# Optimization experiments

Hardware: AMD Instinct MI355X
Metric: run time of the kernel (lower is better)

## Reference

```python
import jax, jax.numpy as jnp
import numpy as np
import math

D_MODEL = 1024
N_HEAD = 16
B, T = 4, 2048


def setup_inputs() -> dict:
    key = jax.random.key(0)
    ks = jax.random.split(key, 12)
    s = 1.0 / math.sqrt(D_MODEL)
    inp = {
        "q": jax.random.normal(ks[0], (B, T, D_MODEL), dtype=jnp.float32),
        "k": jax.random.normal(ks[1], (B, T, D_MODEL), dtype=jnp.float32),
        "v": jax.random.normal(ks[2], (B, T, D_MODEL), dtype=jnp.float32),
        "Wq": jax.random.uniform(ks[3], (D_MODEL, D_MODEL), jnp.float32, -s, s),
        "bq": jax.random.uniform(ks[4], (D_MODEL,), jnp.float32, -s, s),
        "Wk": jax.random.uniform(ks[5], (D_MODEL, D_MODEL), jnp.float32, -s, s),
        "bk": jax.random.uniform(ks[6], (D_MODEL,), jnp.float32, -s, s),
        "Wv": jax.random.uniform(ks[7], (D_MODEL, D_MODEL), jnp.float32, -s, s),
        "bv": jax.random.uniform(ks[8], (D_MODEL,), jnp.float32, -s, s),
        "Wo": jax.random.uniform(ks[9], (D_MODEL, D_MODEL), jnp.float32, -s, s),
        "bo": jax.random.uniform(ks[10], (D_MODEL,), jnp.float32, -s, s),
    }
    return inp


def reference(q, k, v, Wq, bq, Wk, bk, Wv, bv, Wo, bo):
    # NOTE: original module applies all three projections to `q` (k, v args unused)
    batch, time, dim = q.shape
    n_d = dim // N_HEAD
    # torch Linear: x @ W.T + b
    Q = (q @ Wq.T + bq).reshape(batch, time, N_HEAD, n_d).transpose(0, 2, 1, 3)
    K = (q @ Wk.T + bk).reshape(batch, time, N_HEAD, n_d).transpose(0, 2, 1, 3)
    V = (q @ Wv.T + bv).reshape(batch, time, N_HEAD, n_d).transpose(0, 2, 1, 3)
    # [B, H, T, T]
    score = jnp.einsum("bhqd,bhkd->bhqk", Q, K) / jnp.sqrt(jnp.float32(n_d))
    causal = jnp.tril(jnp.ones((time, time), dtype=bool))
    score = jnp.where(causal, score, -jnp.inf)
    # original uses Softmax(dim=-2): normalizes over the QUERY axis (faithful)
    attn = jax.nn.softmax(score, axis=-2)
    ctx = jnp.einsum("bhqk,bhkd->bhqd", attn, V)
    ctx = ctx.transpose(0, 2, 1, 3).reshape(batch, time, dim)
    return ctx @ Wo.T + bo
```

## Files before the change

### kernel.cpp

```cpp
#include <hip/hip_runtime.h>
#include <hip/hip_bf16.h>
#include <cstdint>
#include <cstddef>

typedef __bf16 bf16x8 __attribute__((ext_vector_type(8)));
typedef __bf16 bf16x4 __attribute__((ext_vector_type(4)));
typedef __bf16 bf16x2 __attribute__((ext_vector_type(2)));
typedef float  f32x4  __attribute__((ext_vector_type(4)));

static constexpr int TSEQ  = 2048;
static constexpr int DM    = 1024;
static constexpr int NH    = 16;
static constexpr int HD    = 64;
static constexpr int BATCH = 4;
static constexpr float SCL = 0.18033688011112042f;

__device__ __forceinline__ void gload16(const __bf16* g, __bf16* l) {
  __builtin_amdgcn_global_load_lds((const __attribute__((address_space(1))) void*)g,
                                   (__attribute__((address_space(3))) void*)l, 16, 0, 0);
}

__global__ __launch_bounds__(256) void cvt_kernel(const float* __restrict__ in,
                                                  __bf16* __restrict__ out, int n4) {
  int i = blockIdx.x * 256 + threadIdx.x;
  if (i < n4) {
    float4 v = reinterpret_cast<const float4*>(in)[i];
    bf16x4 o;
    o[0] = (__bf16)v.x; o[1] = (__bf16)v.y; o[2] = (__bf16)v.z; o[3] = (__bf16)v.w;
    reinterpret_cast<bf16x4*>(out)[i] = o;
  }
}

__global__ __launch_bounds__(256) void cvt4_kernel(
    const float* __restrict__ a, const float* __restrict__ bsrc,
    const float* __restrict__ c, const float* __restrict__ d,
    __bf16* __restrict__ oa, __bf16* __restrict__ ob,
    __bf16* __restrict__ oc, __bf16* __restrict__ od, int n4) {
  const float* src = (blockIdx.y == 0) ? a : (blockIdx.y == 1) ? bsrc
                    : (blockIdx.y == 2) ? c : d;
  __bf16* dst = (blockIdx.y == 0) ? oa : (blockIdx.y == 1) ? ob
               : (blockIdx.y == 2) ? oc : od;
  int i = blockIdx.x * 256 + threadIdx.x;
  if (i < n4) {
    float4 v = reinterpret_cast<const float4*>(src)[i];
    bf16x4 o;
    o[0] = (__bf16)v.x; o[1] = (__bf16)v.y; o[2] = (__bf16)v.z; o[3] = (__bf16)v.w;
    reinterpret_cast<bf16x4*>(dst)[i] = o;
  }
}

template <typename OUT_T>
__device__ __forceinline__ void gemm_body(
    const __bf16* __restrict__ A, const __bf16* __restrict__ W,
    const float* __restrict__ bias, OUT_T* __restrict__ C,
    int i0, int o0, __bf16* lA, __bf16* lB) {
  const int tid = threadIdx.x;
  const int w = tid >> 6, l = tid & 63, lr = l & 15, lg = l >> 4;
  const int wr = w >> 1, wc = w & 1;

  f32x4 acc[4][4];
  const f32x4 fzero = {0.f, 0.f, 0.f, 0.f};
#pragma unroll
  for (int mi = 0; mi < 4; ++mi)
#pragma unroll
    for (int ni = 0; ni < 4; ++ni) acc[mi][ni] = fzero;

  for (int kt = 0; kt < 16; ++kt) {
    const int k0 = kt * 64;
#pragma unroll
    for (int n = 0; n < 4; ++n) {
      const int L = n * 2048 + tid * 8;
      const int r = L >> 6, c = L & 63;
      gload16(A + (size_t)(i0 + r) * DM + k0 + c, lA + n * 2048 + w * 512);
      gload16(W + (size_t)(o0 + r) * DM + k0 + c, lB + n * 2048 + w * 512);
    }
    asm volatile("s_waitcnt vmcnt(0)" ::: "memory");
    __syncthreads();
#pragma unroll
    for (int ks = 0; ks < 2; ++ks) {
      bf16x8 af[4], bff[4];
#pragma unroll
      for (int mi = 0; mi < 4; ++mi)
        af[mi] = *(const bf16x8*)(lA + (wr * 64 + mi * 16 + lr) * 64 + ks * 32 + lg * 8);
#pragma unroll
      for (int ni = 0; ni < 4; ++ni)
        bff[ni] = *(const bf16x8*)(lB + (wc * 64 + ni * 16 + lr) * 64 + ks * 32 + lg * 8);
#pragma unroll
      for (int mi = 0; mi < 4; ++mi)
#pragma unroll
        for (int ni = 0; ni < 4; ++ni)
          acc[mi][ni] = __builtin_amdgcn_mfma_f32_16x16x32_bf16(af[mi], bff[ni],
                                                                acc[mi][ni], 0, 0, 0);
    }
    __syncthreads();
  }

#pragma unroll
  for (int ni = 0; ni < 4; ++ni) {
    int col = o0 + wc * 64 + ni * 16 + lr;
    float bb = bias[col];
#pragma unroll
    for (int mi = 0; mi < 4; ++mi) {
      int row = i0 + wr * 64 + mi * 16 + lg * 4;
#pragma unroll
      for (int r = 0; r < 4; ++r)
        C[(size_t)(row + r) * DM + col] = (OUT_T)(acc[mi][ni][r] + bb);
    }
  }
}

__global__ __launch_bounds__(256) void gemm_qkv_kernel(
    const __bf16* __restrict__ A,
    const __bf16* __restrict__ W0, const __bf16* __restrict__ W1,
    const __bf16* __restrict__ W2,
    const float* __restrict__ b0, const float* __restrict__ b1,
    const float* __restrict__ b2,
    __bf16* __restrict__ O0, __bf16* __restrict__ O1, __bf16* __restrict__ O2) {
  __shared__ __align__(16) __bf16 lA[128 * 64];
  __shared__ __align__(16) __bf16 lB[128 * 64];
  const int flat = blockIdx.x;
  const int x = flat & 7, p = flat >> 3;
  const int bx = x * 8 + (p & 7);
  const int by = (p >> 3) & 7;
  const int z = p >> 6;
  const __bf16* W = (z == 0) ? W0 : (z == 1) ? W1 : W2;
  const float* bias = (z == 0) ? b0 : (z == 1) ? b1 : b2;
  __bf16* C = (z == 0) ? O0 : (z == 1) ? O1 : O2;
  gemm_body<__bf16>(A, W, bias, C, bx * 128, by * 128, lA, lB);
}

__global__ __launch_bounds__(256) void gemm_out_kernel(
    const __bf16* __restrict__ A, const __bf16* __restrict__ W,
    const float* __restrict__ bias, float* __restrict__ C) {
  __shared__ __align__(16) __bf16 lA[128 * 64];
  __shared__ __align__(16) __bf16 lB[128 * 64];
  const int flat = blockIdx.x;
  const int x = flat & 7, p = flat >> 3;
  const int bx = x * 8 + (p & 7);
  const int by = p >> 3;
  gemm_body<float>(A, W, bias, C, bx * 128, by * 128, lA, lB);
}

__global__ __launch_bounds__(256) void colstats_kernel(
    const __bf16* __restrict__ Q, const __bf16* __restrict__ K,
    const __bf16* __restrict__ V, __bf16* __restrict__ VT) {
  const int flat = blockIdx.x;
  const int wid = (flat & 7) * 128 + (flat >> 3);
  const int g = wid >> 4, bx = wid & 15;
  const int h = g & 15, b = g >> 4;
  const int tid = threadIdx.x;
  const int w = tid >> 6, l = tid & 63, lr = l & 15, lg = l >> 4;
  const size_t base = (size_t)b * TSEQ * DM + (size_t)h * HD;

  __shared__ float part[4][64];
  __shared__ float invc[64];

  for (int ph = 0; ph < 2; ++ph) {
    const int kt = ph ? (31 - bx) : bx;
    const int k0 = kt * 64;

    bf16x8 kf[4][2];
#pragma unroll
    for (int ct = 0; ct < 4; ++ct)
#pragma unroll
      for (int ks = 0; ks < 2; ++ks)
        kf[ct][ks] = *(const bf16x8*)(K + base + (size_t)(k0 + ct * 16 + lr) * DM +
                                      ks * 32 + lg * 8);

    float csum[4] = {0.f, 0.f, 0.f, 0.f};
    const int nchunks = (TSEQ - k0) >> 4;
    for (int jj = w; jj < nchunks; jj += 4) {
      int qrow = k0 + jj * 16;
      bf16x8 a0 = *(const bf16x8*)(Q + base + (size_t)(qrow + lr) * DM + lg * 8);
      bf16x8 a1 = *(const bf16x8*)(Q + base + (size_t)(qrow + lr) * DM + 32 + lg * 8);
      const bool interior = (jj >= 4);
#pragma unroll
      for (int ct = 0; ct < 4; ++ct) {
        f32x4 s = {0.f, 0.f, 0.f, 0.f};
        s = __builtin_amdgcn_mfma_f32_16x16x32_bf16(a0, kf[ct][0], s, 0, 0, 0);
        s = __builtin_amdgcn_mfma_f32_16x16x32_bf16(a1, kf[ct][1], s, 0, 0, 0);
        if (interior) {
#pragma unroll
          for (int r = 0; r < 4; ++r) csum[ct] += __builtin_amdgcn_exp2f(s[r] * SCL);
        } else {
#pragma unroll
          for (int r = 0; r < 4; ++r) {
            int ql = jj * 16 + lg * 4 + r;
            int kl = ct * 16 + lr;
            float e = __builtin_amdgcn_exp2f(s[r] * SCL);
            csum[ct] += (ql >= kl) ? e : 0.f;
          }
        }
      }
    }

#pragma unroll
    for (int ct = 0; ct < 4; ++ct) {
      csum[ct] += __shfl_xor(csum[ct], 16, 64);
      csum[ct] += __shfl_xor(csum[ct], 32, 64);
    }

    if (l < 16) {
#pragma unroll
      for (int ct = 0; ct < 4; ++ct) part[w][ct * 16 + l] = csum[ct];
    }
    __syncthreads();
    if (tid < 64) {
      float c = part[0][tid] + part[1][tid] + part[2][tid] + part[3][tid];
      invc[tid] = 1.0f / c;
    }
    __syncthreads();

    const int d = tid >> 2, gq = tid & 3;
    size_t vtb = (((size_t)(b * NH + h)) * HD + d) * TSEQ + k0 + gq * 16;
#pragma unroll
    for (int kc = 0; kc < 16; kc += 2) {
      int kl = gq * 16 + kc;
      float v0 = (float)V[base + (size_t)(k0 + kl) * DM + d] * invc[kl];
      float v1 = (float)V[base + (size_t)(k0 + kl + 1) * DM + d] * invc[kl + 1];
      bf16x2 o; o[0] = (__bf16)v0; o[1] = (__bf16)v1;
      *(bf16x2*)(VT + vtb + kc) = o;
    }
    __syncthreads();
  }
}

__device__ __forceinline__ int swz(int e) { return e ^ (((e >> 6) & 7) << 3); }

__global__ __launch_bounds__(256) void ctx_kernel(
    const __bf16* __restrict__ Q, const __bf16* __restrict__ K,
    const __bf16* __restrict__ VT, __bf16* __restrict__ CTX) {
  __shared__ __align__(16) __bf16 lK[4096];
  __shared__ __align__(16) __bf16 lV[4096];
  __shared__ __align__(16) __bf16 lP[4][16 * 88];
  const int flat = blockIdx.x;
  const int wid = (flat & 7) * 128 + (flat >> 3);
  const int g = wid >> 4, bx = wid & 15;
  const int h = g & 15, b = g >> 4;
  const int tid = threadIdx.x;
  const int w = tid >> 6, l = tid & 63, lr = l & 15, lg = l >> 4;
  const size_t base = (size_t)b * TSEQ * DM + (size_t)h * HD;
  const size_t vtb = ((size_t)(b * NH + h)) * HD * TSEQ;
  __bf16* pw = &lP[w][0];

  const int srow = w * 8 + (l >> 3);
  const int scol = (((l & 7) ^ (l >> 3)) << 3);

  for (int ph = 0; ph < 2; ++ph) {
    const int qt = ph ? bx : 31 - bx;
    const int q0 = qt * 64;

    bf16x8 qf[2];
#pragma unroll
    for (int ks = 0; ks < 2; ++ks)
      qf[ks] = *(const bf16x8*)(Q + base + (size_t)(q0 + w * 16 + lr) * DM + ks * 32 + lg * 8);

    f32x4 acc[4];
    const f32x4 fzero = {0.f, 0.f, 0.f, 0.f};
#pragma unroll
    for (int dt = 0; dt < 4; ++dt) acc[dt] = fzero;

    for (int kt = 0; kt <= qt; ++kt) {
      const int k0 = kt * 64;
#pragma unroll
      for (int n = 0; n < 2; ++n) {
        gload16(K + base + (size_t)(k0 + n * 32 + srow) * DM + scol,
                lK + n * 2048 + w * 512);
        gload16(VT + vtb + (size_t)(n * 32 + srow) * TSEQ + k0 + scol,
                lV + n * 2048 + w * 512);
      }
      asm volatile("s_waitcnt vmcnt(0)" ::: "memory");
      __syncthreads();

      const bool diag = (kt == qt);
#pragma unroll
      for (int ct = 0; ct < 4; ++ct) {
        f32x4 s = {0.f, 0.f, 0.f, 0.f};
#pragma unroll
        for (int ks = 0; ks < 2; ++ks) {
          int e = (ct * 16 + lr) * 64 + ks * 32 + lg * 8;
          bf16x8 kb8 = *(const bf16x8*)(lK + swz(e));
          s = __builtin_amdgcn_mfma_f32_16x16x32_bf16(kb8, qf[ks], s, 0, 0, 0);
        }
        bf16x4 pk;
        if (diag) {
#pragma unroll
          for (int r = 0; r < 4; ++r) {
            int ql = w * 16 + lr;
            int kl = ct * 16 + lg * 4 + r;
            float pv = (ql >= kl) ? __builtin_amdgcn_exp2f(s[r] * SCL) : 0.f;
            pk[r] = (__bf16)pv;
          }
        } else {
#pragma unroll
          for (int r = 0; r < 4; ++r)
            pk[r] = (__bf16)__builtin_amdgcn_exp2f(s[r] * SCL);
        }
        *(bf16x4*)(pw + lr * 88 + ct * 16 + lg * 4) = pk;
      }
      asm volatile("" ::: "memory");

      bf16x8 pa[2];
#pragma unroll
      for (int ks = 0; ks < 2; ++ks)
        pa[ks] = *(const bf16x8*)(pw + lr * 88 + ks * 32 + lg * 8);
#pragma unroll
      for (int dt = 0; dt < 4; ++dt) {
#pragma unroll
        for (int ks = 0; ks < 2; ++ks) {
          int e = (dt * 16 + lr) * 64 + ks * 32 + lg * 8;
          bf16x8 vb8 = *(const bf16x8*)(lV + swz(e));
          acc[dt] = __builtin_amdgcn_mfma_f32_16x16x32_bf16(pa[ks], vb8, acc[dt], 0, 0, 0);
        }
      }
      __syncthreads();
    }

#pragma unroll
    for (int dt = 0; dt < 4; ++dt)
#pragma unroll
      for (int r = 0; r < 4; ++r)
        CTX[base + (size_t)(q0 + w * 16 + lg * 4 + r) * DM + dt * 16 + lr] = (__bf16)acc[dt][r];
  }
}

extern "C" void kernel_launch(void* const* d_in, const int* in_sizes, int n_in,
                              void* d_out, int out_size, void* d_ws, size_t ws_size,
                              hipStream_t stream) {
  const float* q  = (const float*)d_in[0];
  const float* Wq = (const float*)d_in[3];
  const float* bq = (const float*)d_in[4];
  const float* Wk = (const float*)d_in[5];
  const float* bk = (const float*)d_in[6];
  const float* Wv = (const float*)d_in[7];
  const float* bv = (const float*)d_in[8];
  const float* Wo = (const float*)d_in[9];
  const float* bo = (const float*)d_in[10];
  float* out = (float*)d_out;

  const size_t NTOK = (size_t)BATCH * TSEQ;
  char* ws = (char*)d_ws;
  __bf16* qb  = (__bf16*)ws; ws += NTOK * DM * 2;
  __bf16* Wqb = (__bf16*)ws; ws += (size_t)DM * DM * 2;
  __bf16* Wkb = (__bf16*)ws; ws += (size_t)DM * DM * 2;
  __bf16* Wvb = (__bf16*)ws; ws += (size_t)DM * DM * 2;
  __bf16* Wob = (__bf16*)ws; ws += (size_t)DM * DM * 2;
  __bf16* Qp  = (__bf16*)ws; ws += NTOK * DM * 2;
  __bf16* Kp  = (__bf16*)ws; ws += NTOK * DM * 2;
  __bf16* Vp  = (__bf16*)ws; ws += NTOK * DM * 2;
  __bf16* VT  = (__bf16*)ws; ws += (size_t)BATCH * NH * HD * TSEQ * 2;
  __bf16* CTX = qb;

  const int nq4 = (int)(NTOK * DM / 4);
  const int nw4 = DM * DM / 4;
  cvt_kernel<<<(nq4 + 255) / 256, 256, 0, stream>>>(q, qb, nq4);
  cvt4_kernel<<<dim3((nw4 + 255) / 256, 4), 256, 0, stream>>>(
      Wq, Wk, Wv, Wo, Wqb, Wkb, Wvb, Wob, nw4);

  gemm_qkv_kernel<<<1536, 256, 0, stream>>>(qb, Wqb, Wkb, Wvb, bq, bk, bv,
                                            Qp, Kp, Vp);

  colstats_kernel<<<1024, 256, 0, stream>>>(Qp, Kp, Vp, VT);
  ctx_kernel<<<1024, 256, 0, stream>>>(Qp, Kp, VT, CTX);

  gemm_out_kernel<<<512, 256, 0, stream>>>(CTX, Wob, bo, out);
}
```

Baseline: 233.2 us.

## Double-buffer projection GEMMs with swizzled LDS, larger tiles and 8 waves

Rewrites the shared GEMM body used by the QKV and output projections. The block tile grows to 128x256 with 8 waves, and LDS stores use an XOR swizzle to avoid bank conflicts. The next K-tile is prefetched into a second LDS buffer while the current one feeds MFMAs, so global loads overlap compute, and s_setprio raises priority around the MFMA blocks. The cost is more LDS per block (96KB), which may limit occupancy, and half as many blocks per launch.

```diff
diff --git a/kernel.cpp b/kernel.cpp
--- a/kernel.cpp
+++ b/kernel.cpp
@@ -50,13 +50,14 @@
 }
 
 template <typename OUT_T>
-__device__ __forceinline__ void gemm_body(
+__device__ __forceinline__ void gemm_body2(
     const __bf16* __restrict__ A, const __bf16* __restrict__ W,
     const float* __restrict__ bias, OUT_T* __restrict__ C,
     int i0, int o0, __bf16* lA, __bf16* lB) {
   const int tid = threadIdx.x;
-  const int w = tid >> 6, l = tid & 63, lr = l & 15, lg = l >> 4;
-  const int wr = w >> 1, wc = w & 1;
+  const int l = tid & 63, lr = l & 15, lg = l >> 4;
+  const int w = tid >> 6;
+  const int wr = w >> 2, wc = w & 3;
 
   f32x4 acc[4][4];
   const f32x4 fzero = {0.f, 0.f, 0.f, 0.f};
@@ -65,34 +66,101 @@
 #pragma unroll
     for (int ni = 0; ni < 4; ++ni) acc[mi][ni] = fzero;
 
-  for (int kt = 0; kt < 16; ++kt) {
-    const int k0 = kt * 64;
+  const int s_row = tid >> 3;
+  const int s_cc  = tid & 7;
+
+  const int NT = DM / 64;
+
+  {
+#pragma unroll
+    for (int n = 0; n < 2; ++n) {
+      int row = n * 64 + s_row;
+      gload16(A + (size_t)(i0 + row) * DM + ((s_cc ^ (row & 7)) << 3),
+              lA + n * 4096 + tid * 8);
+    }
 #pragma unroll
     for (int n = 0; n < 4; ++n) {
-      const int L = n * 2048 + tid * 8;
-      const int r = L >> 6, c = L & 63;
-      gload16(A + (size_t)(i0 + r) * DM + k0 + c, lA + n * 2048 + w * 512);
-      gload16(W + (size_t)(o0 + r) * DM + k0 + c, lB + n * 2048 + w * 512);
-    }
-    asm volatile("s_waitcnt vmcnt(0)" ::: "memory");
-    __syncthreads();
-#pragma unroll
-    for (int ks = 0; ks < 2; ++ks) {
-      bf16x8 af[4], bff[4];
-#pragma unroll
-      for (int mi = 0; mi < 4; ++mi)
-        af[mi] = *(const bf16x8*)(lA + (wr * 64 + mi * 16 + lr) * 64 + ks * 32 + lg * 8);
-#pragma unroll
-      for (int ni = 0; ni < 4; ++ni)
-        bff[ni] = *(const bf16x8*)(lB + (wc * 64 + ni * 16 + lr) * 64 + ks * 32 + lg * 8);
-#pragma unroll
-      for (int mi = 0; mi < 4; ++mi)
-#pragma unroll
-        for (int ni = 0; ni < 4; ++ni)
-          acc[mi][ni] = __builtin_amdgcn_mfma_f32_16x16x32_bf16(af[mi], bff[ni],
-                                                                acc[mi][ni], 0, 0, 0);
-    }
-    __syncthreads();
+      int row = n * 64 + s_row;
+      gload16(W + (size_t)(o0 + row) * DM + ((s_cc ^ (row & 7)) << 3),
+              lB + n * 4096 + tid * 8);
+    }
+  }
+  asm volatile("s_waitcnt vmcnt(0)" ::: "memory");
+  __syncthreads();
+
+  for (int t = 0; t < NT; ++t) {
+    const int cur = t & 1;
+    if (t + 1 < NT) {
+      const int k0 = (t + 1) * 64;
+      const int nxt = cur ^ 1;
+#pragma unroll
+      for (int n = 0; n < 2; ++n) {
+        int row = n * 64 + s_row;
+        gload16(A + (size_t)(i0 + row) * DM + k0 + ((s_cc ^ (row & 7)) << 3),
+                lA + nxt * 8192 + n * 4096 + tid * 8);
+      }
+#pragma unroll
+      for (int n = 0; n < 4; ++n) {
+        int row = n * 64 + s_row;
+        gload16(W + (size_t)(o0 + row) * DM + k0 + ((s_cc ^ (row & 7)) << 3),
+                lB + nxt * 16384 + n * 4096 + tid * 8);
+      }
+    }
+
+    const __bf16* cA = lA + cur * 8192;
+    const __bf16* cB = lB + cur * 16384;
+
+    bf16x8 af[4][2], bf_[2][2];
+#pragma unroll
+    for (int mi = 0; mi < 4; ++mi)
+#pragma unroll
+      for (int ks = 0; ks < 2; ++ks) {
+        int row = wr * 64 + mi * 16 + lr;
+        int chunk = (ks * 4 + lg) ^ (row & 7);
+        af[mi][ks] = *(const bf16x8*)(cA + row * 64 + chunk * 8);
+      }
+#pragma unroll
+    for (int ni = 0; ni < 2; ++ni)
+#pragma unroll
+      for (int ks = 0; ks < 2; ++ks) {
+        int row = wc * 64 + ni * 16 + lr;
+        int chunk = (ks * 4 + lg) ^ (row & 7);
+        bf_[ni][ks] = *(const bf16x8*)(cB + row * 64 + chunk * 8);
+      }
+    __builtin_amdgcn_s_setprio(1);
+#pragma unroll
+    for (int mi = 0; mi < 4; ++mi)
+#pragma unroll
+      for (int ni = 0; ni < 2; ++ni)
+#pragma unroll
+        for (int ks = 0; ks < 2; ++ks)
+          acc[mi][ni] = __builtin_amdgcn_mfma_f32_16x16x32_bf16(
+              af[mi][ks], bf_[ni][ks], acc[mi][ni], 0, 0, 0);
+    __builtin_amdgcn_s_setprio(0);
+
+#pragma unroll
+    for (int ni = 0; ni < 2; ++ni)
+#pragma unroll
+      for (int ks = 0; ks < 2; ++ks) {
+        int row = wc * 64 + (ni + 2) * 16 + lr;
+        int chunk = (ks * 4 + lg) ^ (row & 7);
+        bf_[ni][ks] = *(const bf16x8*)(cB + row * 64 + chunk * 8);
+      }
+    __builtin_amdgcn_s_setprio(1);
+#pragma unroll
+    for (int mi = 0; mi < 4; ++mi)
+#pragma unroll
+      for (int ni = 0; ni < 2; ++ni)
+#pragma unroll
+        for (int ks = 0; ks < 2; ++ks)
+          acc[mi][ni + 2] = __builtin_amdgcn_mfma_f32_16x16x32_bf16(
+              af[mi][ks], bf_[ni][ks], acc[mi][ni + 2], 0, 0, 0);
+    __builtin_amdgcn_s_setprio(0);
+
+    if (t + 1 < NT) {
+      asm volatile("s_waitcnt vmcnt(0)" ::: "memory");
+      __syncthreads();
+    }
   }
 
 #pragma unroll
@@ -109,36 +177,37 @@
   }
 }
 
-__global__ __launch_bounds__(256) void gemm_qkv_kernel(
+__global__ __launch_bounds__(512, 2) void gemm_qkv_kernel(
     const __bf16* __restrict__ A,
     const __bf16* __restrict__ W0, const __bf16* __restrict__ W1,
     const __bf16* __restrict__ W2,
     const float* __restrict__ b0, const float* __restrict__ b1,
     const float* __restrict__ b2,
     __bf16* __restrict__ O0, __bf16* __restrict__ O1, __bf16* __restrict__ O2) {
-  __shared__ __align__(16) __bf16 lA[128 * 64];
-  __shared__ __align__(16) __bf16 lB[128 * 64];
+  __shared__ __align__(16) __bf16 lA[2 * 128 * 64];
+  __shared__ __align__(16) __bf16 lB[2 * 256 * 64];
   const int flat = blockIdx.x;
-  const int x = flat & 7, p = flat >> 3;
-  const int bx = x * 8 + (p & 7);
-  const int by = (p >> 3) & 7;
-  const int z = p >> 6;
+  const int xcd = flat & 7, idx = flat >> 3;
+  const int mi = xcd * 8 + (idx & 7);
+  const int nig = idx >> 3;
+  const int z = nig >> 2;
+  const int o0 = (nig & 3) * 256;
   const __bf16* W = (z == 0) ? W0 : (z == 1) ? W1 : W2;
   const float* bias = (z == 0) ? b0 : (z == 1) ? b1 : b2;
   __bf16* C = (z == 0) ? O0 : (z == 1) ? O1 : O2;
-  gemm_body<__bf16>(A, W, bias, C, bx * 128, by * 128, lA, lB);
-}
-
-__global__ __launch_bounds__(256) void gemm_out_kernel(
+  gemm_body2<__bf16>(A, W, bias, C, mi * 128, o0, lA, lB);
+}
+
+__global__ __launch_bounds__(512, 2) void gemm_out_kernel(
     const __bf16* __restrict__ A, const __bf16* __restrict__ W,
     const float* __restrict__ bias, float* __restrict__ C) {
-  __shared__ __align__(16) __bf16 lA[128 * 64];
-  __shared__ __align__(16) __bf16 lB[128 * 64];
+  __shared__ __align__(16) __bf16 lA[2 * 128 * 64];
+  __shared__ __align__(16) __bf16 lB[2 * 256 * 64];
   const int flat = blockIdx.x;
-  const int x = flat & 7, p = flat >> 3;
-  const int bx = x * 8 + (p & 7);
-  const int by = p >> 3;
-  gemm_body<float>(A, W, bias, C, bx * 128, by * 128, lA, lB);
+  const int xcd = flat & 7, idx = flat >> 3;
+  const int mi = xcd * 8 + (idx & 7);
+  const int ni = idx >> 3;
+  gemm_body2<float>(A, W, bias, C, mi * 128, ni * 256, lA, lB);
 }
 
 __global__ __launch_bounds__(256) void colstats_kernel(
@@ -357,11 +426,11 @@
   cvt4_kernel<<<dim3((nw4 + 255) / 256, 4), 256, 0, stream>>>(
       Wq, Wk, Wv, Wo, Wqb, Wkb, Wvb, Wob, nw4);
 
-  gemm_qkv_kernel<<<1536, 256, 0, stream>>>(qb, Wqb, Wkb, Wvb, bq, bk, bv,
-                                            Qp, Kp, Vp);
+  gemm_qkv_kernel<<<768, 512, 0, stream>>>(qb, Wqb, Wkb, Wvb, bq, bk, bv,
+                                           Qp, Kp, Vp);
 
   colstats_kernel<<<1024, 256, 0, stream>>>(Qp, Kp, Vp, VT);
   ctx_kernel<<<1024, 256, 0, stream>>>(Qp, Kp, VT, CTX);
 
-  gemm_out_kernel<<<512, 256, 0, stream>>>(CTX, Wob, bo, out);
-}
+  gemm_out_kernel<<<256, 512, 0, stream>>>(CTX, Wob, bo, out);
+}
```

Result: faster. 220.3 us (-5.5%).
